# Kernel optimization log

Measured on AMD Instinct MI355X. Metric: run time of the kernel, lower is better.

The kernel has to match this reference:

```python
import jax, jax.numpy as jnp
import numpy as np

B_, L, HID = 2, 1024, 2048
N, H, P, NA = 128, 64, 64, 32   # state, heads, head_dim, rope angle pairs
DIN = 2 * H * P + 2 * N + 3 * H + NA  # 8672
EPS = 1e-5
A_FLOOR = 1e-4


def setup_inputs() -> dict:
    key = jax.random.key(0)
    k0, k1, k2 = jax.random.split(key, 3)
    hidden_states = jax.random.normal(k0, (B_, L, HID), jnp.float32)
    in_proj_w = jax.random.normal(k1, (DIN, HID), jnp.float32) * 0.02
    out_proj_w = jax.random.normal(k2, (HID, H * P), jnp.float32) * 0.02
    # dt_bias init exactly as in the torch module
    rng = np.random.default_rng(0)
    dt = np.exp(rng.random(H) * (np.log(0.1) - np.log(0.001)) + np.log(0.001))
    dt = np.clip(dt, 1e-4, None)
    dt_bias = jnp.asarray(dt + np.log(-np.expm1(-dt)), jnp.float32)
    return {
        'hidden_states': hidden_states,
        'in_proj_w': in_proj_w,
        'dt_bias': dt_bias,
        'B_bias': jnp.ones((H, N), jnp.float32),
        'C_bias': jnp.ones((H, N), jnp.float32),
        'B_norm_w': jnp.ones((N,), jnp.float32),
        'C_norm_w': jnp.ones((N,), jnp.float32),
        'D': jnp.ones((H,), jnp.float32),
        'out_proj_w': out_proj_w,
    }


def _rmsnorm(x, w):
    var = jnp.mean(jnp.square(x), axis=-1, keepdims=True)
    return x * jax.lax.rsqrt(var + EPS) * w


def _forward(hidden_states, in_proj_w, dt_bias, B_bias, C_bias,
             B_norm_w, C_norm_w, D, out_proj_w):
    b, l, _ = hidden_states.shape
    proj = hidden_states @ in_proj_w.T  # (b,l,DIN)
    splits = np.cumsum([H * P, H * P, N, N, H, H, H])
    z, x, Braw, Craw, dd_dt, dd_A, trap, angles = jnp.split(proj, splits, axis=-1)
    z = z.reshape(b, l, H, P)
    x = x.reshape(b, l, H, P)
    # data-dependent A (per token, per head), clamped
    A = jnp.minimum(-jax.nn.softplus(dd_A.astype(jnp.float32)), -A_FLOOR)
    DT = jax.nn.softplus(dd_dt + dt_bias)          # (b,l,H)
    decay = jnp.exp(A * DT)                        # (b,l,H)
    lam = jax.nn.sigmoid(trap)                     # trapezoidal weight (b,l,H)
    # RMSNorm then per-head input-independent bias (n_groups=1, mimo_rank=1)
    Bn = _rmsnorm(Braw, B_norm_w)[:, :, None, :] + B_bias  # (b,l,H,N)
    Cn = _rmsnorm(Craw, C_norm_w)[:, :, None, :] + C_bias  # (b,l,H,N)
    # blockwise rotary on first 2*NA state dims, cumulative data-dependent phase
    phase = jnp.cumsum(angles[:, :, None, :].astype(jnp.float32) * DT[..., None], axis=1)  # (b,l,H,NA)
    cos, sin = jnp.cos(phase), jnp.sin(phase)

    def rope(v):
        v1, v2, rest = v[..., :NA], v[..., NA:2 * NA], v[..., 2 * NA:]
        return jnp.concatenate([v1 * cos - v2 * sin, v1 * sin + v2 * cos, rest], axis=-1)

    Bh = rope(Bn.astype(jnp.float32))
    Ch = rope(Cn.astype(jnp.float32))
    u = (x * DT[..., None]).astype(jnp.float32)    # (b,l,H,P)

    # selective scan with generalized trapezoidal discretization:
    # h_t = a_t h_{t-1} + (1-lam_t) u_t B_t^T + lam_t a_t u_{t-1} B_{t-1}^T
    def step(carry, inp):
        h, Gp = carry
        Bt, Ct, ut, dec, lm = inp
        G = ut[..., :, None] * Bt[..., None, :]    # (b,H,P,N)
        h = dec[..., None, None] * h + (1.0 - lm)[..., None, None] * G \
            + (lm * dec)[..., None, None] * Gp
        y = jnp.einsum('bhpn,bhn->bhp', h, Ct)
        return (h, G), y

    h0 = jnp.zeros((b, H, P, N), jnp.float32)
    xs = (Bh.transpose(1, 0, 2, 3), Ch.transpose(1, 0, 2, 3),
          u.transpose(1, 0, 2, 3), decay.transpose(1, 0, 2), lam.transpose(1, 0, 2))
    _, ys = jax.lax.scan(step, (h0, h0), xs)       # (l,b,H,P)
    y = ys.transpose(1, 0, 2, 3)
    y = y + D[None, None, :, None] * x             # skip connection
    y = y * jax.nn.silu(z)                         # output gate (Z path in kernel)
    y = y.reshape(b, l, H * P)
    return y @ out_proj_w.T


def reference(hidden_states, in_proj_w, dt_bias, B_bias, C_bias,
              B_norm_w, C_norm_w, D, out_proj_w):
    return _forward(hidden_states, in_proj_w, dt_bias, B_bias, C_bias,
                    B_norm_w, C_norm_w, D, out_proj_w)
```

## Files before the change

### kernel.cpp

```cpp
#include <hip/hip_runtime.h>
#include <hip/hip_bf16.h>
#include <cstdint>
#include <cstddef>

#define DEVINL __device__ __forceinline__

typedef __attribute__((ext_vector_type(8))) short bf16x8;
typedef __attribute__((ext_vector_type(4))) float f32x4;

DEVINL float bf2f(unsigned short u){
  union { unsigned u32; float f; } cv; cv.u32 = ((unsigned)u) << 16; return cv.f;
}
DEVINL unsigned short f2bf(float f){
  union { float f; unsigned u32; } cv; cv.f = f;
  unsigned u = cv.u32;
  return (unsigned short)((u + 0x7FFFu + ((u >> 16) & 1u)) >> 16);
}
DEVINL float softplusf(float x){ return x > 20.f ? x : log1pf(expf(x)); }

DEVINL void g2l16(const void* gptr, void* ldsptr){
  __builtin_amdgcn_global_load_lds(
      (const __attribute__((address_space(1))) unsigned int*)gptr,
      (__attribute__((address_space(3))) unsigned int*)(uintptr_t)ldsptr,
      16, 0, 0);
}

DEVINL int swzb(int row, int col){ return row*256 + ((col*2) ^ ((row&7)<<4)); }
DEVINL void ldsw_write8(unsigned short* b, int row, int col, bf16x8 v){
  *(bf16x8*)((char*)b + swzb(row,col)) = v;
}
DEVINL bf16x8 ldsw_read8(const unsigned short* b, int row, int col){
  return *(const bf16x8*)((const char*)b + swzb(row,col));
}
DEVINL void ldsw_write1(unsigned short* b, int row, int col, unsigned short v){
  *(unsigned short*)((char*)b + swzb(row,col)) = v;
}
DEVINL unsigned short ldsw_read1(const unsigned short* b, int row, int col){
  return *(const unsigned short*)((const char*)b + swzb(row,col));
}

__global__ __launch_bounds__(256) void k_f32_to_bf16(
    const float* __restrict__ in, unsigned short* __restrict__ out, long n)
{
  long i = ((long)blockIdx.x * 256 + threadIdx.x) * 4;
  if (i + 3 < n){
    float4 v = *(const float4*)(in + i);
    unsigned long long pk =
        (unsigned long long)f2bf(v.x)
      | ((unsigned long long)f2bf(v.y) << 16)
      | ((unsigned long long)f2bf(v.z) << 32)
      | ((unsigned long long)f2bf(v.w) << 48);
    *(unsigned long long*)(out + i) = pk;
  }
}

template<bool OUT_BF16>
__global__ __launch_bounds__(256) void k_gemm_bt(
    const unsigned short* __restrict__ A,
    const unsigned short* __restrict__ Bt,
    void* __restrict__ Cout,
    int K, int Nrows, int Npad, int xm, int tmx, int tnx)
{
  __shared__ unsigned short Asub[128*64];
  __shared__ unsigned short Bsub[128*64];
  const int tid = threadIdx.x;
  const int x = blockIdx.x & 7, i = blockIdx.x >> 3;
  const int rt = (x % xm) * tmx + (i % tmx);
  const int ct = (x / xm) * tnx + (i / tmx);
  const int lane = tid & 63, wave = tid >> 6;
  const int wr = wave >> 1, wc = wave & 1;
  const int fr = lane & 15;
  const int fq = lane >> 4;

  const int srow0 = tid >> 3;
  const int sgrp  = (tid & 7) ^ ((tid >> 3) & 7);
  size_t aoff[4], boff[4];
  #pragma unroll
  for (int j = 0; j < 4; j++){
    int row = j*32 + srow0;
    aoff[j] = (size_t)(rt*128 + row) * K + sgrp*8;
    int brow = ct*128 + row; if (brow > Nrows-1) brow = Nrows-1;
    boff[j] = (size_t)brow * K + sgrp*8;
  }

  f32x4 acc[4][4] = {};

  for (int k0 = 0; k0 < K; k0 += 64){
    #pragma unroll
    for (int j = 0; j < 4; j++){
      g2l16(A  + aoff[j] + k0, (char*)Asub + (j*256 + tid)*16);
      g2l16(Bt + boff[j] + k0, (char*)Bsub + (j*256 + tid)*16);
    }
    asm volatile("s_waitcnt vmcnt(0)" ::: "memory");
    __syncthreads();

    #pragma unroll
    for (int kk = 0; kk < 2; kk++){
      bf16x8 af[4], bfr[4];
      const int slot = (kk*4 + fq) ^ (fr & 7);
      #pragma unroll
      for (int j = 0; j < 4; j++){
        int ra = wr*64 + j*16 + fr;
        int rb = wc*64 + j*16 + fr;
        af[j]  = *(const bf16x8*)((const char*)Asub + ra*128 + slot*16);
        bfr[j] = *(const bf16x8*)((const char*)Bsub + rb*128 + slot*16);
      }
      #pragma unroll
      for (int mi = 0; mi < 4; mi++)
        #pragma unroll
        for (int ni = 0; ni < 4; ni++)
          acc[mi][ni] = __builtin_amdgcn_mfma_f32_16x16x32_bf16(af[mi], bfr[ni], acc[mi][ni], 0, 0, 0);
    }
    __syncthreads();
  }

  const int er = (lane >> 4) * 4;
  const int ec = lane & 15;
  #pragma unroll
  for (int mi = 0; mi < 4; mi++){
    #pragma unroll
    for (int ni = 0; ni < 4; ni++){
      const int row = rt*128 + wr*64 + mi*16 + er;
      const int col = ct*128 + wc*64 + ni*16 + ec;
      #pragma unroll
      for (int r = 0; r < 4; r++){
        if (OUT_BF16)
          ((unsigned short*)Cout)[(size_t)(row+r)*Npad + col] = f2bf(acc[mi][ni][r]);
        else
          ((float*)Cout)[(size_t)(row+r)*Npad + col] = acc[mi][ni][r];
      }
    }
  }
}

__global__ __launch_bounds__(128) void k_rmsprep(
    const unsigned short* __restrict__ proj, const float* __restrict__ Bw,
    const float* __restrict__ Cw, const float* __restrict__ dt_bias,
    unsigned short* __restrict__ Bb2, unsigned short* __restrict__ Cb2,
    float* __restrict__ DTt, float* __restrict__ logdec, float* __restrict__ lamt)
{
  int row = blockIdx.x, n = threadIdx.x;
  size_t base = (size_t)row * 8704;
  float bv = bf2f(proj[base + 8192 + n]);
  float cv = bf2f(proj[base + 8320 + n]);
  float sb = bv*bv, sc = cv*cv;
  #pragma unroll
  for (int m = 1; m < 64; m <<= 1){ sb += __shfl_xor(sb, m, 64); sc += __shfl_xor(sc, m, 64); }
  __shared__ float red[4];
  if ((n & 63) == 0){ red[(n>>6)*2] = sb; red[(n>>6)*2+1] = sc; }
  __syncthreads();
  sb = red[0] + red[2];
  sc = red[1] + red[3];
  float rb = rsqrtf(sb*(1.f/128.f) + 1e-5f);
  float rc = rsqrtf(sc*(1.f/128.f) + 1e-5f);
  Bb2[row*128 + n] = f2bf(bv*rb*Bw[n]);
  Cb2[row*128 + n] = f2bf(cv*rc*Cw[n]);
  if (n < 64){
    int h = n, b = row >> 10, l = row & 1023;
    float dd_dt = bf2f(proj[base + 8448 + h]);
    float dd_A  = bf2f(proj[base + 8512 + h]);
    float trap  = bf2f(proj[base + 8576 + h]);
    float DT = softplusf(dd_dt + dt_bias[h]);
    float A  = -fmaxf(softplusf(dd_A), 1e-4f);
    size_t o = ((size_t)(b*64 + h))*1024 + l;
    DTt[o]    = DT;
    logdec[o] = A * DT;
    lamt[o]   = 1.f / (1.f + expf(-trap));
  }
}

__global__ __launch_bounds__(256) void k_phase(
    const unsigned short* __restrict__ proj, const float* __restrict__ DTt,
    const float* __restrict__ logdec, const float* __restrict__ lamt,
    float* __restrict__ clcb, float* __restrict__ gb,
    unsigned short* __restrict__ cosb, unsigned short* __restrict__ sinb)
{
  int bh = blockIdx.x, b = bh >> 6, h = bh & 63;
  int tid = threadIdx.x;
  size_t sbase = (size_t)bh * 1024;
  {
    int e0 = tid * 4;
    float v0 = logdec[sbase+e0], v1 = logdec[sbase+e0+1],
          v2 = logdec[sbase+e0+2], v3 = logdec[sbase+e0+3];
    float p0 = v0, p1 = p0+v1, p2 = p1+v2, p3 = p2+v3;
    float tot = p3;
    int sub = tid & 31;
    float incl = tot;
    #pragma unroll
    for (int off = 1; off < 32; off <<= 1){
      float u = __shfl_up(incl, off, 32);
      if (sub >= off) incl += u;
    }
    float excl = incl - tot;
    clcb[sbase+e0]   = excl + p0;
    clcb[sbase+e0+1] = excl + p1;
    clcb[sbase+e0+2] = excl + p2;
    clcb[sbase+e0+3] = excl + p3;
    #pragma unroll
    for (int q = 0; q < 4; q++){
      int l = e0 + q;
      int ln = (l == 1023) ? 1023 : l + 1;
      gb[sbase+l] = 1.f - lamt[sbase+l] + lamt[sbase+ln];
    }
  }
  int na = tid & 31, c = tid >> 5;
  __shared__ float part[8][32];
  const float* dtr = DTt + sbase;
  float s = 0.f;
  for (int q = 0; q < 128; q++){
    int l = c*128 + q; int row = b*1024 + l;
    float ang = bf2f(proj[(size_t)row*8704 + 8640 + na]);
    s = fmaf(ang, dtr[l], s);
  }
  part[c][na] = s;
  __syncthreads();
  float off = 0.f;
  for (int cc = 0; cc < c; cc++) off += part[cc][na];
  float ph = off;
  for (int q = 0; q < 128; q++){
    int l = c*128 + q; int row = b*1024 + l;
    float ang = bf2f(proj[(size_t)row*8704 + 8640 + na]);
    ph = fmaf(ang, dtr[l], ph);
    float sn, cs;
    __sincosf(ph, &sn, &cs);
    size_t o = ((size_t)row*64 + h)*32 + na;
    cosb[o] = f2bf(cs); sinb[o] = f2bf(sn);
  }
}

__global__ __launch_bounds__(256, 1) void k_intra(
    const unsigned short* __restrict__ proj,
    const unsigned short* __restrict__ Bb2, const unsigned short* __restrict__ Cb2,
    const float* __restrict__ Bbias, const float* __restrict__ Cbias,
    const unsigned short* __restrict__ cosb, const unsigned short* __restrict__ sinb,
    const float* __restrict__ DTt, const float* __restrict__ clcb,
    const float* __restrict__ gb, const float* __restrict__ lamt,
    const float* __restrict__ Dv, unsigned short* __restrict__ ybf,
    unsigned short* __restrict__ Gbuf)
{
  const int c = blockIdx.x & 7, bh = blockIdx.x >> 3;
  const int b = bh >> 6, h = bh & 63;
  const int tid = threadIdx.x, lane = tid & 63, wave = tid >> 6;
  const int wr = wave >> 1, wc = wave & 1;
  const int fr = lane & 15, fq = lane >> 4;

  __shared__ __align__(16) unsigned short Cs[128*128];
  __shared__ __align__(16) unsigned short Bs[128*128];
  __shared__ __align__(16) unsigned short BTs[128*128];
  __shared__ __align__(16) unsigned short Uts[64*128];
  __shared__ float clcs[128], lams[128], gs[128], wUs[128], dts[128];
  __shared__ float biasB[128], biasC[128];

  const int base = b*1024 + c*128;
  const size_t shbase = (size_t)bh * 1024;
  const float Dh = Dv[h];

  if (tid < 128){
    int l = c*128 + tid;
    clcs[tid] = clcb[shbase + l];
    dts[tid]  = DTt[shbase + l];
    lams[tid] = lamt[shbase + l];
    gs[tid]   = gb[shbase + l];
    biasB[tid] = Bbias[h*128 + tid];
  } else {
    biasC[tid-128] = Cbias[h*128 + tid-128];
  }
  __syncthreads();
  if (tid < 128) wUs[tid] = __expf(clcs[127] - clcs[tid]) * gs[tid];

  {
    const int t = tid >> 1, half = tid & 1;
    const int grow = base + t;
    const size_t roff = (size_t)grow*128 + half*64;
    if (half == 0){
      bf16x8 cc[4], sv[4];
      #pragma unroll
      for (int j = 0; j < 4; j++){
        cc[j] = *(const bf16x8*)(cosb + ((size_t)grow*64 + h)*32 + j*8);
        sv[j] = *(const bf16x8*)(sinb + ((size_t)grow*64 + h)*32 + j*8);
      }
      #pragma unroll
      for (int j = 0; j < 4; j++){
        bf16x8 vlo = *(const bf16x8*)(Cb2 + roff + j*8);
        bf16x8 vhi = *(const bf16x8*)(Cb2 + roff + 32 + j*8);
        bf16x8 olo, ohi;
        #pragma unroll
        for (int e = 0; e < 8; e++){
          float a = bf2f((unsigned short)vlo[e]) + biasC[j*8+e];
          float d = bf2f((unsigned short)vhi[e]) + biasC[32+j*8+e];
          float cf = bf2f((unsigned short)cc[j][e]);
          float sf = bf2f((unsigned short)sv[j][e]);
          olo[e] = (short)f2bf(a*cf - d*sf);
          ohi[e] = (short)f2bf(a*sf + d*cf);
        }
        ldsw_write8(Cs, t, j*8, olo);
        ldsw_write8(Cs, t, 32 + j*8, ohi);
      }
      #pragma unroll
      for (int j = 0; j < 4; j++){
        bf16x8 vlo = *(const bf16x8*)(Bb2 + roff + j*8);
        bf16x8 vhi = *(const bf16x8*)(Bb2 + roff + 32 + j*8);
        bf16x8 olo, ohi;
        #pragma unroll
        for (int e = 0; e < 8; e++){
          float a = bf2f((unsigned short)vlo[e]) + biasB[j*8+e];
          float d = bf2f((unsigned short)vhi[e]) + biasB[32+j*8+e];
          float cf = bf2f((unsigned short)cc[j][e]);
          float sf = bf2f((unsigned short)sv[j][e]);
          olo[e] = (short)f2bf(a*cf - d*sf);
          ohi[e] = (short)f2bf(a*sf + d*cf);
        }
        ldsw_write8(Bs, t, j*8, olo);
        ldsw_write8(Bs, t, 32 + j*8, ohi);
        #pragma unroll
        for (int e = 0; e < 8; e++){
          ldsw_write1(BTs, j*8+e, t, (unsigned short)olo[e]);
          ldsw_write1(BTs, 32+j*8+e, t, (unsigned short)ohi[e]);
        }
      }
    } else {
      #pragma unroll
      for (int j = 0; j < 8; j++){
        bf16x8 v = *(const bf16x8*)(Cb2 + roff + j*8);
        bf16x8 o;
        #pragma unroll
        for (int e = 0; e < 8; e++) o[e] = (short)f2bf(bf2f((unsigned short)v[e]) + biasC[64+j*8+e]);
        ldsw_write8(Cs, t, 64 + j*8, o);
      }
      #pragma unroll
      for (int j = 0; j < 8; j++){
        bf16x8 v = *(const bf16x8*)(Bb2 + roff + j*8);
        bf16x8 o;
        #pragma unroll
        for (int e = 0; e < 8; e++) o[e] = (short)f2bf(bf2f((unsigned short)v[e]) + biasB[64+j*8+e]);
        ldsw_write8(Bs, t, 64 + j*8, o);
        #pragma unroll
        for (int e = 0; e < 8; e++) ldsw_write1(BTs, 64+j*8+e, t, (unsigned short)o[e]);
      }
    }
  }
  {
    const int p = tid & 63, jg = tid >> 6;
    #pragma unroll 4
    for (int q = 0; q < 32; q++){
      int j = jg*32 + q;
      size_t pb = (size_t)(base + j) * 8704;
      float xx = bf2f(proj[pb + 4096 + h*64 + p]);
      ldsw_write1(Uts, p, j, f2bf(xx * dts[j]));
    }
  }
  __syncthreads();

  f32x4 acc1[4][4];
  #pragma unroll
  for (int mi = 0; mi < 4; mi++)
    #pragma unroll
    for (int ni = 0; ni < 4; ni++)
      acc1[mi][ni] = (f32x4){0.f,0.f,0.f,0.f};
  #pragma unroll
  for (int ks = 0; ks < 4; ks++){
    bf16x8 af[4], bj[4];
    #pragma unroll
    for (int mi = 0; mi < 4; mi++) af[mi] = ldsw_read8(Cs, wr*64+mi*16+fr, ks*32+fq*8);
    #pragma unroll
    for (int ni = 0; ni < 4; ni++) bj[ni] = ldsw_read8(Bs, wc*64+ni*16+fr, ks*32+fq*8);
    #pragma unroll
    for (int mi = 0; mi < 4; mi++)
      #pragma unroll
      for (int ni = 0; ni < 4; ni++)
        acc1[mi][ni] = __builtin_amdgcn_mfma_f32_16x16x32_bf16(af[mi], bj[ni], acc1[mi][ni], 0,0,0);
  }
  unsigned short pr[4][4][4];
  int jj[4]; float clcj[4], gj[4];
  #pragma unroll
  for (int ni = 0; ni < 4; ni++){ jj[ni] = wc*64+ni*16+fr; clcj[ni] = clcs[jj[ni]]; gj[ni] = gs[jj[ni]]; }
  #pragma unroll
  for (int mi = 0; mi < 4; mi++){
    #pragma unroll
    for (int r = 0; r < 4; r++){
      int t = wr*64+mi*16+fq*4+r;
      float ct_ = clcs[t], lt = lams[t];
      #pragma unroll
      for (int ni = 0; ni < 4; ni++){
        int j = jj[ni];
        float w = (j < t) ? __expf(ct_ - clcj[ni])*gj[ni] : ((j == t) ? (1.f - lt) : 0.f);
        pr[mi][ni][r] = f2bf(acc1[mi][ni][r] * w);
      }
    }
  }
  __syncthreads();
  #pragma unroll
  for (int mi = 0; mi < 4; mi++)
    #pragma unroll
    for (int ni = 0; ni < 4; ni++)
      #pragma unroll
      for (int r = 0; r < 4; r++)
        ldsw_write1(Bs, wr*64+mi*16+fq*4+r, wc*64+ni*16+fr, pr[mi][ni][r]);
  __syncthreads();

  f32x4 acc2[4][2];
  #pragma unroll
  for (int mi = 0; mi < 4; mi++)
    #pragma unroll
    for (int ni = 0; ni < 2; ni++)
      acc2[mi][ni] = (f32x4){0.f,0.f,0.f,0.f};
  #pragma unroll
  for (int ks = 0; ks < 4; ks++){
    bf16x8 af[4], uj[2];
    #pragma unroll
    for (int mi = 0; mi < 4; mi++) af[mi] = ldsw_read8(Bs, wr*64+mi*16+fr, ks*32+fq*8);
    #pragma unroll
    for (int ni = 0; ni < 2; ni++) uj[ni] = ldsw_read8(Uts, wc*32+ni*16+fr, ks*32+fq*8);
    #pragma unroll
    for (int mi = 0; mi < 4; mi++)
      #pragma unroll
      for (int ni = 0; ni < 2; ni++)
        acc2[mi][ni] = __builtin_amdgcn_mfma_f32_16x16x32_bf16(af[mi], uj[ni], acc2[mi][ni], 0,0,0);
  }
  f32x4 accS[2][4];
  #pragma unroll
  for (int mi = 0; mi < 2; mi++)
    #pragma unroll
    for (int ni = 0; ni < 4; ni++)
      accS[mi][ni] = (f32x4){0.f,0.f,0.f,0.f};
  #pragma unroll
  for (int ks = 0; ks < 4; ks++){
    bf16x8 au[2], bn[4];
    #pragma unroll
    for (int mi = 0; mi < 2; mi++){
      bf16x8 raw = ldsw_read8(Uts, wr*32+mi*16+fr, ks*32+fq*8);
      #pragma unroll
      for (int e = 0; e < 8; e++){
        float f = bf2f((unsigned short)raw[e]) * wUs[ks*32+fq*8+e];
        au[mi][e] = (short)f2bf(f);
      }
    }
    #pragma unroll
    for (int ni = 0; ni < 4; ni++) bn[ni] = ldsw_read8(BTs, wc*64+ni*16+fr, ks*32+fq*8);
    #pragma unroll
    for (int mi = 0; mi < 2; mi++)
      #pragma unroll
      for (int ni = 0; ni < 4; ni++)
        accS[mi][ni] = __builtin_amdgcn_mfma_f32_16x16x32_bf16(au[mi], bn[ni], accS[mi][ni], 0,0,0);
  }

  #pragma unroll
  for (int mi = 0; mi < 4; mi++){
    #pragma unroll
    for (int ni = 0; ni < 2; ni++){
      #pragma unroll
      for (int r = 0; r < 4; r++){
        int t = wr*64+mi*16+fq*4+r;
        int p = wc*32+ni*16+fr;
        float xv = bf2f(ldsw_read1(Uts, p, t)) / fmaxf(dts[t], 1e-30f);
        float o = acc2[mi][ni][r] + Dh*xv;
        ybf[(size_t)(base + t)*4096 + h*64 + p] = f2bf(o);
      }
    }
  }
  #pragma unroll
  for (int mi = 0; mi < 2; mi++)
    #pragma unroll
    for (int ni = 0; ni < 4; ni++)
      #pragma unroll
      for (int r = 0; r < 4; r++){
        int p = wr*32+mi*16+fq*4+r;
        int n = wc*64+ni*16+fr;
        Gbuf[(size_t)blockIdx.x*8192 + p*128 + n] = f2bf(accS[mi][ni][r]);
      }
}

__global__ __launch_bounds__(256) void k_scanstate(
    const float* __restrict__ clcb, unsigned short* __restrict__ Gbuf)
{
  const int bh = blockIdx.x, tid = threadIdx.x;
  float S[32];
  #pragma unroll
  for (int q = 0; q < 32; q++) S[q] = 0.f;
  const size_t gbase = (size_t)bh*65536 + (size_t)tid*32;
  for (int c = 0; c < 8; c++){
    float decEnd = __expf(clcb[(size_t)bh*1024 + c*128 + 127]);
    unsigned short* p = Gbuf + gbase + (size_t)c*8192;
    bf16x8 g[4], s[4];
    #pragma unroll
    for (int q = 0; q < 4; q++) g[q] = *(const bf16x8*)(p + q*8);
    #pragma unroll
    for (int q = 0; q < 4; q++)
      #pragma unroll
      for (int e = 0; e < 8; e++) s[q][e] = (short)f2bf(S[q*8+e]);
    #pragma unroll
    for (int q = 0; q < 4; q++) *(bf16x8*)(p + q*8) = s[q];
    #pragma unroll
    for (int q = 0; q < 4; q++)
      #pragma unroll
      for (int e = 0; e < 8; e++)
        S[q*8+e] = decEnd*S[q*8+e] + bf2f((unsigned short)g[q][e]);
  }
}

__global__ __launch_bounds__(256) void k_inter(
    const unsigned short* __restrict__ proj,
    const unsigned short* __restrict__ Cb2, const float* __restrict__ Cbias,
    const unsigned short* __restrict__ cosb, const unsigned short* __restrict__ sinb,
    const float* __restrict__ clcb, const unsigned short* __restrict__ Sprev,
    unsigned short* __restrict__ ybf)
{
  const int c = blockIdx.x & 7, bh = blockIdx.x >> 3;
  const int b = bh >> 6, h = bh & 63;
  const int tid = threadIdx.x, lane = tid & 63, wave = tid >> 6;
  const int wr = wave >> 1, wc = wave & 1;
  const int fr = lane & 15, fq = lane >> 4;

  __shared__ __align__(16) unsigned short Cs[128*128];
  __shared__ __align__(16) unsigned short Ss[64*128];
  __shared__ float expclcs[128], biasC[128];

  const int base = b*1024 + c*128;

  if (tid < 128){
    expclcs[tid] = __expf(clcb[(size_t)bh*1024 + c*128 + tid]);
    biasC[tid] = Cbias[h*128 + tid];
  }
  __syncthreads();

  {
    const int t = tid >> 1, half = tid & 1;
    const int grow = base + t;
    const size_t roff = (size_t)grow*128 + half*64;
    if (half == 0){
      bf16x8 cc[4], sv[4];
      #pragma unroll
      for (int j = 0; j < 4; j++){
        cc[j] = *(const bf16x8*)(cosb + ((size_t)grow*64 + h)*32 + j*8);
        sv[j] = *(const bf16x8*)(sinb + ((size_t)grow*64 + h)*32 + j*8);
      }
      #pragma unroll
      for (int j = 0; j < 4; j++){
        bf16x8 vlo = *(const bf16x8*)(Cb2 + roff + j*8);
        bf16x8 vhi = *(const bf16x8*)(Cb2 + roff + 32 + j*8);
        bf16x8 olo, ohi;
        #pragma unroll
        for (int e = 0; e < 8; e++){
          float a = bf2f((unsigned short)vlo[e]) + biasC[j*8+e];
          float d = bf2f((unsigned short)vhi[e]) + biasC[32+j*8+e];
          float cf = bf2f((unsigned short)cc[j][e]);
          float sf = bf2f((unsigned short)sv[j][e]);
          olo[e] = (short)f2bf(a*cf - d*sf);
          ohi[e] = (short)f2bf(a*sf + d*cf);
        }
        ldsw_write8(Cs, t, j*8, olo);
        ldsw_write8(Cs, t, 32 + j*8, ohi);
      }
    } else {
      #pragma unroll
      for (int j = 0; j < 8; j++){
        bf16x8 v = *(const bf16x8*)(Cb2 + roff + j*8);
        bf16x8 o;
        #pragma unroll
        for (int e = 0; e < 8; e++) o[e] = (short)f2bf(bf2f((unsigned short)v[e]) + biasC[64+j*8+e]);
        ldsw_write8(Cs, t, 64 + j*8, o);
      }
    }
  }
  {
    const unsigned short* src = Sprev + (size_t)blockIdx.x*8192 + (size_t)tid*32;
    #pragma unroll
    for (int j = 0; j < 4; j++){
      bf16x8 v = *(const bf16x8*)(src + j*8);
      int f = tid*32 + j*8;
      ldsw_write8(Ss, f >> 7, f & 127, v);
    }
  }
  __syncthreads();

  f32x4 acc[4][2];
  #pragma unroll
  for (int mi = 0; mi < 4; mi++)
    #pragma unroll
    for (int ni = 0; ni < 2; ni++)
      acc[mi][ni] = (f32x4){0.f,0.f,0.f,0.f};
  #pragma unroll
  for (int ks = 0; ks < 4; ks++){
    bf16x8 af[4], sj[2];
    #pragma unroll
    for (int mi = 0; mi < 4; mi++) af[mi] = ldsw_read8(Cs, wr*64+mi*16+fr, ks*32+fq*8);
    #pragma unroll
    for (int ni = 0; ni < 2; ni++) sj[ni] = ldsw_read8(Ss, wc*32+ni*16+fr, ks*32+fq*8);
    #pragma unroll
    for (int mi = 0; mi < 4; mi++)
      #pragma unroll
      for (int ni = 0; ni < 2; ni++)
        acc[mi][ni] = __builtin_amdgcn_mfma_f32_16x16x32_bf16(af[mi], sj[ni], acc[mi][ni], 0,0,0);
  }

  #pragma unroll
  for (int mi = 0; mi < 4; mi++){
    #pragma unroll
    for (int ni = 0; ni < 2; ni++){
      #pragma unroll
      for (int r = 0; r < 4; r++){
        int t = wr*64+mi*16+fq*4+r;
        int p = wc*32+ni*16+fr;
        size_t yoff = (size_t)(base + t)*4096 + h*64 + p;
        float y = bf2f(ybf[yoff]) + expclcs[t]*acc[mi][ni][r];
        float zv = bf2f(proj[(size_t)(base + t)*8704 + h*64 + p]);
        float sl = zv / (1.f + __expf(-zv));
        ybf[yoff] = f2bf(y * sl);
      }
    }
  }
}

extern "C" void kernel_launch(void* const* d_in, const int* in_sizes, int n_in,
                              void* d_out, int out_size, void* d_ws, size_t ws_size,
                              hipStream_t stream)
{
  const float* hs    = (const float*)d_in[0];
  const float* w1    = (const float*)d_in[1];
  const float* dtb   = (const float*)d_in[2];
  const float* Bbias = (const float*)d_in[3];
  const float* Cbias = (const float*)d_in[4];
  const float* Bw    = (const float*)d_in[5];
  const float* Cw    = (const float*)d_in[6];
  const float* Dv    = (const float*)d_in[7];
  const float* wo    = (const float*)d_in[8];
  float* out = (float*)d_out;
  char* ws = (char*)d_ws;

  unsigned short* projbf = (unsigned short*)(ws + 0UL);
  unsigned short* W1bf   = (unsigned short*)(ws + 35651584UL);
  unsigned short* Gbuf   = W1bf;
  unsigned short* Wobf   = W1bf;
  unsigned short* ybf    = (unsigned short*)(ws + 52428800UL);
  unsigned short* hsbf   = (unsigned short*)(ws + 71172096UL);
  unsigned short* cosb   = hsbf;
  unsigned short* sinb   = (unsigned short*)(ws + 79560704UL);
  float* DTt    = (float*)(ws + 87949312UL);
  float* logdec = (float*)(ws + 88473600UL);
  float* lamt   = (float*)(ws + 88997888UL);
  float* clcb   = (float*)(ws + 89522176UL);
  float* gb     = (float*)(ws + 90046464UL);
  unsigned short* Bb2 = (unsigned short*)(ws + 90570752UL);
  unsigned short* Cb2 = (unsigned short*)(ws + 91095040UL);
  if (ws_size < 91619328UL) return;

  (void)in_sizes; (void)n_in; (void)out_size;

  k_f32_to_bf16<<<17344, 256, 0, stream>>>(w1, W1bf, 17760256L);
  k_f32_to_bf16<<<4096,  256, 0, stream>>>(hs, hsbf, 4194304L);
  k_gemm_bt<true><<<1088, 256, 0, stream>>>(hsbf, W1bf, projbf, 2048, 8672, 8704, 2, 8, 17);
  k_rmsprep<<<2048, 128, 0, stream>>>(projbf, Bw, Cw, dtb, Bb2, Cb2, DTt, logdec, lamt);
  k_phase<<<128, 256, 0, stream>>>(projbf, DTt, logdec, lamt, clcb, gb, cosb, sinb);
  k_intra<<<1024, 256, 0, stream>>>(projbf, Bb2, Cb2, Bbias, Cbias,
                                    cosb, sinb, DTt, clcb, gb, lamt, Dv, ybf, Gbuf);
  k_scanstate<<<128, 256, 0, stream>>>(clcb, Gbuf);
  k_inter<<<1024, 256, 0, stream>>>(projbf, Cb2, Cbias, cosb, sinb, clcb, Gbuf, ybf);
  k_f32_to_bf16<<<8192, 256, 0, stream>>>(wo, Wobf, 8388608L);
  k_gemm_bt<false><<<256, 256, 0, stream>>>(ybf, Wobf, out, 4096, 2048, 2048, 4, 4, 8);
}
```

Measured before the change: 331.3 us.

## Widen intra-chunk kernel to 512 threads and merge the two input bf16 conversions

The intra-chunk SSM kernel now runs 8 waves per block instead of 4. The MFMA tiles are split across a 2x4 wave grid, and the B/C rotary preparation and U staging are spread across four thread roles per row. This raises per-block parallelism and cuts the per-wave accumulator count. The two f32-to-bf16 conversion launches for the weights and hidden states are fused into one launch that picks its source by block index, saving a kernel launch. The risks are higher register pressure at the 512-thread launch bound and more barrier participants.

New measurement: 332.7 us. Within noise of the previous version (+0.4%).

```diff
diff --git a/kernel.cpp b/kernel.cpp
--- a/kernel.cpp
+++ b/kernel.cpp
@@ -37,6 +37,25 @@
 }
 DEVINL unsigned short ldsw_read1(const unsigned short* b, int row, int col){
   return *(const unsigned short*)((const char*)b + swzb(row,col));
+}
+
+__global__ __launch_bounds__(256) void k_conv2(
+    const float* __restrict__ a, unsigned short* __restrict__ oa, long na, int nba,
+    const float* __restrict__ b, unsigned short* __restrict__ ob, long nb)
+{
+  const float* in; unsigned short* out; long n; long blk;
+  if ((int)blockIdx.x < nba){ in = a; out = oa; n = na; blk = blockIdx.x; }
+  else                      { in = b; out = ob; n = nb; blk = blockIdx.x - nba; }
+  long i = (blk * 256 + threadIdx.x) * 4;
+  if (i + 3 < n){
+    float4 v = *(const float4*)(in + i);
+    unsigned long long pk =
+        (unsigned long long)f2bf(v.x)
+      | ((unsigned long long)f2bf(v.y) << 16)
+      | ((unsigned long long)f2bf(v.z) << 32)
+      | ((unsigned long long)f2bf(v.w) << 48);
+    *(unsigned long long*)(out + i) = pk;
+  }
 }
 
 __global__ __launch_bounds__(256) void k_f32_to_bf16(
@@ -228,7 +247,7 @@
   }
 }
 
-__global__ __launch_bounds__(256, 1) void k_intra(
+__global__ __launch_bounds__(512, 1) void k_intra(
     const unsigned short* __restrict__ proj,
     const unsigned short* __restrict__ Bb2, const unsigned short* __restrict__ Cb2,
     const float* __restrict__ Bbias, const float* __restrict__ Cbias,
@@ -241,7 +260,7 @@
   const int c = blockIdx.x & 7, bh = blockIdx.x >> 3;
   const int b = bh >> 6, h = bh & 63;
   const int tid = threadIdx.x, lane = tid & 63, wave = tid >> 6;
-  const int wr = wave >> 1, wc = wave & 1;
+  const int wr = wave >> 2, wc = wave & 3;
   const int fr = lane & 15, fq = lane >> 4;
 
   __shared__ __align__(16) unsigned short Cs[128*128];
@@ -262,17 +281,17 @@
     lams[tid] = lamt[shbase + l];
     gs[tid]   = gb[shbase + l];
     biasB[tid] = Bbias[h*128 + tid];
-  } else {
+  } else if (tid < 256){
     biasC[tid-128] = Cbias[h*128 + tid-128];
   }
   __syncthreads();
   if (tid < 128) wUs[tid] = __expf(clcs[127] - clcs[tid]) * gs[tid];
 
   {
-    const int t = tid >> 1, half = tid & 1;
+    const int t = tid >> 2, q = tid & 3;
     const int grow = base + t;
-    const size_t roff = (size_t)grow*128 + half*64;
-    if (half == 0){
+    const size_t roff = (size_t)grow*128;
+    if (q == 0){
       bf16x8 cc[4], sv[4];
       #pragma unroll
       for (int j = 0; j < 4; j++){
@@ -296,6 +315,22 @@
         ldsw_write8(Cs, t, j*8, olo);
         ldsw_write8(Cs, t, 32 + j*8, ohi);
       }
+    } else if (q == 1){
+      #pragma unroll
+      for (int j = 0; j < 8; j++){
+        bf16x8 v = *(const bf16x8*)(Cb2 + roff + 64 + j*8);
+        bf16x8 o;
+        #pragma unroll
+        for (int e = 0; e < 8; e++) o[e] = (short)f2bf(bf2f((unsigned short)v[e]) + biasC[64+j*8+e]);
+        ldsw_write8(Cs, t, 64 + j*8, o);
+      }
+    } else if (q == 2){
+      bf16x8 cc[4], sv[4];
+      #pragma unroll
+      for (int j = 0; j < 4; j++){
+        cc[j] = *(const bf16x8*)(cosb + ((size_t)grow*64 + h)*32 + j*8);
+        sv[j] = *(const bf16x8*)(sinb + ((size_t)grow*64 + h)*32 + j*8);
+      }
       #pragma unroll
       for (int j = 0; j < 4; j++){
         bf16x8 vlo = *(const bf16x8*)(Bb2 + roff + j*8);
@@ -321,15 +356,7 @@
     } else {
       #pragma unroll
       for (int j = 0; j < 8; j++){
-        bf16x8 v = *(const bf16x8*)(Cb2 + roff + j*8);
-        bf16x8 o;
-        #pragma unroll
-        for (int e = 0; e < 8; e++) o[e] = (short)f2bf(bf2f((unsigned short)v[e]) + biasC[64+j*8+e]);
-        ldsw_write8(Cs, t, 64 + j*8, o);
-      }
-      #pragma unroll
-      for (int j = 0; j < 8; j++){
-        bf16x8 v = *(const bf16x8*)(Bb2 + roff + j*8);
+        bf16x8 v = *(const bf16x8*)(Bb2 + roff + 64 + j*8);
         bf16x8 o;
         #pragma unroll
         for (int e = 0; e < 8; e++) o[e] = (short)f2bf(bf2f((unsigned short)v[e]) + biasB[64+j*8+e]);
@@ -342,8 +369,8 @@
   {
     const int p = tid & 63, jg = tid >> 6;
     #pragma unroll 4
-    for (int q = 0; q < 32; q++){
-      int j = jg*32 + q;
+    for (int q = 0; q < 16; q++){
+      int j = jg*16 + q;
       size_t pb = (size_t)(base + j) * 8704;
       float xx = bf2f(proj[pb + 4096 + h*64 + p]);
       ldsw_write1(Uts, p, j, f2bf(xx * dts[j]));
@@ -351,29 +378,29 @@
   }
   __syncthreads();
 
-  f32x4 acc1[4][4];
+  f32x4 acc1[4][2];
   #pragma unroll
   for (int mi = 0; mi < 4; mi++)
     #pragma unroll
-    for (int ni = 0; ni < 4; ni++)
+    for (int ni = 0; ni < 2; ni++)
       acc1[mi][ni] = (f32x4){0.f,0.f,0.f,0.f};
   #pragma unroll
   for (int ks = 0; ks < 4; ks++){
-    bf16x8 af[4], bj[4];
+    bf16x8 af[4], bj[2];
     #pragma unroll
     for (int mi = 0; mi < 4; mi++) af[mi] = ldsw_read8(Cs, wr*64+mi*16+fr, ks*32+fq*8);
     #pragma unroll
-    for (int ni = 0; ni < 4; ni++) bj[ni] = ldsw_read8(Bs, wc*64+ni*16+fr, ks*32+fq*8);
+    for (int ni = 0; ni < 2; ni++) bj[ni] = ldsw_read8(Bs, wc*32+ni*16+fr, ks*32+fq*8);
     #pragma unroll
     for (int mi = 0; mi < 4; mi++)
       #pragma unroll
-      for (int ni = 0; ni < 4; ni++)
+      for (int ni = 0; ni < 2; ni++)
         acc1[mi][ni] = __builtin_amdgcn_mfma_f32_16x16x32_bf16(af[mi], bj[ni], acc1[mi][ni], 0,0,0);
   }
-  unsigned short pr[4][4][4];
-  int jj[4]; float clcj[4], gj[4];
-  #pragma unroll
-  for (int ni = 0; ni < 4; ni++){ jj[ni] = wc*64+ni*16+fr; clcj[ni] = clcs[jj[ni]]; gj[ni] = gs[jj[ni]]; }
+  unsigned short pr[4][2][4];
+  int jj[2]; float clcj[2], gj[2];
+  #pragma unroll
+  for (int ni = 0; ni < 2; ni++){ jj[ni] = wc*32+ni*16+fr; clcj[ni] = clcs[jj[ni]]; gj[ni] = gs[jj[ni]]; }
   #pragma unroll
   for (int mi = 0; mi < 4; mi++){
     #pragma unroll
@@ -381,7 +408,7 @@
       int t = wr*64+mi*16+fq*4+r;
       float ct_ = clcs[t], lt = lams[t];
       #pragma unroll
-      for (int ni = 0; ni < 4; ni++){
+      for (int ni = 0; ni < 2; ni++){
         int j = jj[ni];
         float w = (j < t) ? __expf(ct_ - clcj[ni])*gj[ni] : ((j == t) ? (1.f - lt) : 0.f);
         pr[mi][ni][r] = f2bf(acc1[mi][ni][r] * w);
@@ -392,40 +419,34 @@
   #pragma unroll
   for (int mi = 0; mi < 4; mi++)
     #pragma unroll
-    for (int ni = 0; ni < 4; ni++)
+    for (int ni = 0; ni < 2; ni++)
       #pragma unroll
       for (int r = 0; r < 4; r++)
-        ldsw_write1(Bs, wr*64+mi*16+fq*4+r, wc*64+ni*16+fr, pr[mi][ni][r]);
-  __syncthreads();
-
-  f32x4 acc2[4][2];
-  #pragma unroll
-  for (int mi = 0; mi < 4; mi++)
+        ldsw_write1(Bs, wr*64+mi*16+fq*4+r, wc*32+ni*16+fr, pr[mi][ni][r]);
+  __syncthreads();
+
+  f32x4 acc2[4];
+  #pragma unroll
+  for (int mi = 0; mi < 4; mi++) acc2[mi] = (f32x4){0.f,0.f,0.f,0.f};
+  #pragma unroll
+  for (int ks = 0; ks < 4; ks++){
+    bf16x8 af[4], uj;
+    #pragma unroll
+    for (int mi = 0; mi < 4; mi++) af[mi] = ldsw_read8(Bs, wr*64+mi*16+fr, ks*32+fq*8);
+    uj = ldsw_read8(Uts, wc*16+fr, ks*32+fq*8);
+    #pragma unroll
+    for (int mi = 0; mi < 4; mi++)
+      acc2[mi] = __builtin_amdgcn_mfma_f32_16x16x32_bf16(af[mi], uj, acc2[mi], 0,0,0);
+  }
+  f32x4 accS[2][2];
+  #pragma unroll
+  for (int mi = 0; mi < 2; mi++)
     #pragma unroll
     for (int ni = 0; ni < 2; ni++)
-      acc2[mi][ni] = (f32x4){0.f,0.f,0.f,0.f};
+      accS[mi][ni] = (f32x4){0.f,0.f,0.f,0.f};
   #pragma unroll
   for (int ks = 0; ks < 4; ks++){
-    bf16x8 af[4], uj[2];
-    #pragma unroll
-    for (int mi = 0; mi < 4; mi++) af[mi] = ldsw_read8(Bs, wr*64+mi*16+fr, ks*32+fq*8);
-    #pragma unroll
-    for (int ni = 0; ni < 2; ni++) uj[ni] = ldsw_read8(Uts, wc*32+ni*16+fr, ks*32+fq*8);
-    #pragma unroll
-    for (int mi = 0; mi < 4; mi++)
-      #pragma unroll
-      for (int ni = 0; ni < 2; ni++)
-        acc2[mi][ni] = __builtin_amdgcn_mfma_f32_16x16x32_bf16(af[mi], uj[ni], acc2[mi][ni], 0,0,0);
-  }
-  f32x4 accS[2][4];
-  #pragma unroll
-  for (int mi = 0; mi < 2; mi++)
-    #pragma unroll
-    for (int ni = 0; ni < 4; ni++)
-      accS[mi][ni] = (f32x4){0.f,0.f,0.f,0.f};
-  #pragma unroll
-  for (int ks = 0; ks < 4; ks++){
-    bf16x8 au[2], bn[4];
+    bf16x8 au[2], bn[2];
     #pragma unroll
     for (int mi = 0; mi < 2; mi++){
       bf16x8 raw = ldsw_read8(Uts, wr*32+mi*16+fr, ks*32+fq*8);
@@ -436,36 +457,33 @@
       }
     }
     #pragma unroll
-    for (int ni = 0; ni < 4; ni++) bn[ni] = ldsw_read8(BTs, wc*64+ni*16+fr, ks*32+fq*8);
+    for (int ni = 0; ni < 2; ni++) bn[ni] = ldsw_read8(BTs, wc*32+ni*16+fr, ks*32+fq*8);
     #pragma unroll
     for (int mi = 0; mi < 2; mi++)
       #pragma unroll
-      for (int ni = 0; ni < 4; ni++)
+      for (int ni = 0; ni < 2; ni++)
         accS[mi][ni] = __builtin_amdgcn_mfma_f32_16x16x32_bf16(au[mi], bn[ni], accS[mi][ni], 0,0,0);
   }
 
   #pragma unroll
   for (int mi = 0; mi < 4; mi++){
     #pragma unroll
-    for (int ni = 0; ni < 2; ni++){
-      #pragma unroll
-      for (int r = 0; r < 4; r++){
-        int t = wr*64+mi*16+fq*4+r;
-        int p = wc*32+ni*16+fr;
-        float xv = bf2f(ldsw_read1(Uts, p, t)) / fmaxf(dts[t], 1e-30f);
-        float o = acc2[mi][ni][r] + Dh*xv;
-        ybf[(size_t)(base + t)*4096 + h*64 + p] = f2bf(o);
-      }
+    for (int r = 0; r < 4; r++){
+      int t = wr*64+mi*16+fq*4+r;
+      int p = wc*16+fr;
+      float xv = bf2f(ldsw_read1(Uts, p, t)) / fmaxf(dts[t], 1e-30f);
+      float o = acc2[mi][r] + Dh*xv;
+      ybf[(size_t)(base + t)*4096 + h*64 + p] = f2bf(o);
     }
   }
   #pragma unroll
   for (int mi = 0; mi < 2; mi++)
     #pragma unroll
-    for (int ni = 0; ni < 4; ni++)
+    for (int ni = 0; ni < 2; ni++)
       #pragma unroll
       for (int r = 0; r < 4; r++){
         int p = wr*32+mi*16+fq*4+r;
-        int n = wc*64+ni*16+fr;
+        int n = wc*32+ni*16+fr;
         Gbuf[(size_t)blockIdx.x*8192 + p*128 + n] = f2bf(accS[mi][ni][r]);
       }
 }
@@ -646,12 +664,11 @@
 
   (void)in_sizes; (void)n_in; (void)out_size;
 
-  k_f32_to_bf16<<<17344, 256, 0, stream>>>(w1, W1bf, 17760256L);
-  k_f32_to_bf16<<<4096,  256, 0, stream>>>(hs, hsbf, 4194304L);
+  k_conv2<<<21440, 256, 0, stream>>>(w1, W1bf, 17760256L, 17344, hs, hsbf, 4194304L);
   k_gemm_bt<true><<<1088, 256, 0, stream>>>(hsbf, W1bf, projbf, 2048, 8672, 8704, 2, 8, 17);
   k_rmsprep<<<2048, 128, 0, stream>>>(projbf, Bw, Cw, dtb, Bb2, Cb2, DTt, logdec, lamt);
   k_phase<<<128, 256, 0, stream>>>(projbf, DTt, logdec, lamt, clcb, gb, cosb, sinb);
-  k_intra<<<1024, 256, 0, stream>>>(projbf, Bb2, Cb2, Bbias, Cbias,
+  k_intra<<<1024, 512, 0, stream>>>(projbf, Bb2, Cb2, Bbias, Cbias,
                                     cosb, sinb, DTt, clcb, gb, lamt, Dv, ybf, Gbuf);
   k_scanstate<<<128, 256, 0, stream>>>(clcb, Gbuf);
   k_inter<<<1024, 256, 0, stream>>>(projbf, Cb2, Cbias, cosb, sinb, clcb, Gbuf, ybf);
```
